# Kernel optimization log

Measured on AMD Instinct MI355X. Metric: run time of the kernel, lower is better.

Reference implementation:

```python
import jax, jax.numpy as jnp
import numpy as np

NUM_FEATURES = 128   # conv spatial length
WINDOW = 128         # conv channels / lstm seq len
KC = 16              # kernels per group
KS = 3               # conv kernel size
FC1 = 32             # number of independent LSTMs
H = 32               # lstm hidden size
NL = 2               # lstm layers
PAD = 1
POOL_LEN = (NUM_FEATURES + 2 * PAD) // 2  # maxpool(k=2,s=2,p=1) output length
B = 128


def setup_inputs():
    key = jax.random.key(0)
    ks = jax.random.split(key, 13)
    x = jax.random.normal(ks[0], (B, WINDOW, NUM_FEATURES), jnp.float32)
    conv_w = jax.random.normal(ks[1], (WINDOW * KC, 1, KS), jnp.float32) * 0.3
    conv_b = jax.random.normal(ks[2], (WINDOW * KC,), jnp.float32) * 0.1
    fc1_in = KC * POOL_LEN
    fc1_w = jax.random.normal(ks[3], (FC1, fc1_in), jnp.float32) * 0.02
    fc1_b = jax.random.normal(ks[4], (FC1,), jnp.float32) * 0.02
    w_ih0 = jax.random.normal(ks[5], (FC1, 4 * H), jnp.float32) * 0.1          # layer0, input size 1
    w_ih1 = jax.random.normal(ks[6], (NL - 1, FC1, 4 * H, H), jnp.float32) * 0.1
    w_hh = jax.random.normal(ks[7], (NL, FC1, 4 * H, H), jnp.float32) * 0.1
    b_lstm = jax.random.normal(ks[8], (NL, FC1, 4 * H), jnp.float32) * 0.1     # bias_ih + bias_hh combined
    mu_w = jax.random.normal(ks[9], (1, FC1 * H), jnp.float32) * 0.05
    mu_b = jax.random.normal(ks[10], (1,), jnp.float32) * 0.05
    lv_w = jax.random.normal(ks[11], (1, FC1 * H), jnp.float32) * 0.05
    lv_b = jax.random.normal(ks[12], (1,), jnp.float32) * 0.05
    return {"x": x, "conv_w": conv_w, "conv_b": conv_b, "fc1_w": fc1_w, "fc1_b": fc1_b,
            "w_ih0": w_ih0, "w_ih1": w_ih1, "w_hh": w_hh, "b_lstm": b_lstm,
            "mu_w": mu_w, "mu_b": mu_b, "lv_w": lv_w, "lv_b": lv_b}


def _lstm_cell(gates, c_prev):
    # torch gate order: i, f, g, o
    i, f, g, o = jnp.split(gates, 4, axis=-1)
    c_new = jax.nn.sigmoid(f) * c_prev + jax.nn.sigmoid(i) * jnp.tanh(g)
    h_new = jax.nn.sigmoid(o) * jnp.tanh(c_new)
    return h_new, c_new


def reference(x, conv_w, conv_b, fc1_w, fc1_b, w_ih0, w_ih1, w_hh, b_lstm, mu_w, mu_b, lv_w, lv_b):
    bsz = x.shape[0]
    # grouped conv1d: groups = WINDOW, each group maps 1 -> KC channels
    y = jax.lax.conv_general_dilated(x, conv_w, window_strides=(1,), padding=[(PAD, PAD)],
                                     feature_group_count=WINDOW,
                                     dimension_numbers=('NCH', 'OIH', 'NCH'))
    y = jax.nn.relu(y + conv_b[None, :, None])
    neg = jnp.finfo(y.dtype).min
    y = jnp.pad(y, ((0, 0), (0, 0), (PAD, PAD)), constant_values=neg)
    y = y.reshape(bsz, WINDOW * KC, POOL_LEN, 2).max(axis=-1)
    # regroup to [B, WINDOW, KC*POOL_LEN] (channel layout = group-major, matches torch view)
    y = y.reshape(bsz, WINDOW, KC * POOL_LEN)
    z = jnp.einsum('bwi,oi->bwo', y, fc1_w) + fc1_b   # [B, WINDOW, FC1]

    # FC1 independent NL-layer LSTMs batched over the feature axis; time axis = WINDOW
    h0 = jnp.zeros((NL, bsz, FC1, H), z.dtype)
    c0 = jnp.zeros_like(h0)

    def step(carry, x_t):  # x_t: [B, FC1]
        h, c = carry
        hs, cs = [], []
        gates = jnp.einsum('bf,fg->bfg', x_t, w_ih0) + jnp.einsum('bfh,fgh->bfg', h[0], w_hh[0]) + b_lstm[0]
        h_l, c_l = _lstm_cell(gates, c[0])
        hs.append(h_l); cs.append(c_l)
        for l in range(1, NL):
            gates = (jnp.einsum('bfh,fgh->bfg', h_l, w_ih1[l - 1])
                     + jnp.einsum('bfh,fgh->bfg', h[l], w_hh[l]) + b_lstm[l])
            h_l, c_l = _lstm_cell(gates, c[l])
            hs.append(h_l); cs.append(c_l)
        return (jnp.stack(hs), jnp.stack(cs)), None

    (h_fin, _), _ = jax.lax.scan(step, (h0, c0), jnp.transpose(z, (1, 0, 2)))
    combined = h_fin[-1].reshape(bsz, FC1 * H)  # top layer, last step; feature-major like torch.cat
    mu = combined @ mu_w.T + mu_b
    log_var = combined @ lv_w.T + lv_b
    sigma = jnp.exp(0.5 * log_var)
    return (mu - 1.96 * sigma, mu, mu + 1.96 * sigma, log_var)
```

## Files before the change

### kernel.cpp

```cpp
#include <hip/hip_runtime.h>
#include <hip/hip_bf16.h>
#include <math.h>

#define BATCH 128
#define WIN   128
#define NF    128
#define KC    16
#define POOL  65
#define NFC1  32
#define HS    32
#define LW    40
#define KP    1056
#define PSTR  1064

typedef float f32x4 __attribute__((ext_vector_type(4)));
typedef short bf16x8 __attribute__((ext_vector_type(8)));

#define LOG2E   1.442695041f
#define LOG2E2  2.885390082f

__device__ __forceinline__ float cellf(float& c, float gi, float gf, float gg, float go) {
    float ei = __builtin_amdgcn_exp2f(gi);
    float ef = __builtin_amdgcn_exp2f(gf);
    float eg = __builtin_amdgcn_exp2f(gg);
    float eo = __builtin_amdgcn_exp2f(go);
    float sf = __builtin_amdgcn_rcpf(1.f + ef);
    c = fmaf(sf, c, (eg - 1.f) * __builtin_amdgcn_rcpf((1.f + ei) * (eg + 1.f)));
    float ec = __builtin_amdgcn_exp2f(__builtin_amdgcn_fmed3f(c, -30.f, 30.f) * LOG2E2);
    return (ec - 1.f) * __builtin_amdgcn_rcpf((1.f + eo) * (ec + 1.f));
}
__device__ __forceinline__ unsigned short f2bf(float x) {
    __hip_bfloat16 h = __float2bfloat16(x);
    unsigned short u; __builtin_memcpy(&u, &h, 2); return u;
}
__device__ __forceinline__ float bf2f(unsigned short u) {
    unsigned int v = ((unsigned int)u) << 16;
    float f; __builtin_memcpy(&f, &v, 4); return f;
}
__device__ __forceinline__ bf16x8 load_row8_scaled(const float* row, float sc) {
    float4 lo = ((const float4*)row)[0];
    float4 hi = ((const float4*)row)[1];
    union { bf16x8 v; unsigned short u[8]; } t;
    t.u[0] = f2bf(lo.x * sc); t.u[1] = f2bf(lo.y * sc); t.u[2] = f2bf(lo.z * sc); t.u[3] = f2bf(lo.w * sc);
    t.u[4] = f2bf(hi.x * sc); t.u[5] = f2bf(hi.y * sc); t.u[6] = f2bf(hi.z * sc); t.u[7] = f2bf(hi.w * sc);
    return t.v;
}

__global__ __launch_bounds__(256) void k0_wconv(
    const float* __restrict__ fc1_w, unsigned short* __restrict__ w_bf)
{
    const int o = blockIdx.x;
    for (int i = threadIdx.x; i < KP; i += 256) {
        float v = (i < KC * POOL) ? fc1_w[(size_t)o * (KC * POOL) + i] : 0.f;
        w_bf[(size_t)o * KP + i] = f2bf(v);
    }
}

__global__ __launch_bounds__(128, 2) void k1_conv_fc1(
    const float* __restrict__ x, const float* __restrict__ conv_w, const float* __restrict__ conv_b,
    const unsigned short* __restrict__ w_bf, const float* __restrict__ fc1_b, float* __restrict__ z)
{
    __shared__ __align__(16) unsigned short xp[16][132];
    __shared__ __align__(16) unsigned short poolb[16 * PSTR];
    __shared__ float cw[KC][3];
    __shared__ float cb[KC];
    __shared__ float fb[NFC1];

    const int w = blockIdx.x >> 3;
    const int bbase = (blockIdx.x & 7) * 16;
    const int tid = threadIdx.x;

    if (tid < KC * 3) cw[tid / 3][tid % 3] = conv_w[(w * KC + tid / 3) * 3 + tid % 3];
    if (tid >= 64 && tid < 64 + KC) cb[tid - 64] = conv_b[w * KC + (tid - 64)];
    if (tid >= 96 && tid < 96 + NFC1) fb[tid - 96] = fc1_b[tid - 96];

    for (int i = tid; i < 16 * 32; i += 128) {
        int b = i >> 5, q = i & 31;
        float4 v = ((const float4*)(x + (size_t)(bbase + b) * (WIN * NF) + (size_t)w * NF))[q];
        unsigned short* dst = &xp[b][1 + q * 4];
        dst[0] = f2bf(v.x); dst[1] = f2bf(v.y); dst[2] = f2bf(v.z); dst[3] = f2bf(v.w);
    }
    if (tid < 16) { xp[tid][0] = 0; xp[tid][129] = 0; xp[tid][130] = 0; xp[tid][131] = 0; }
    __syncthreads();

    {
        const int b0 = tid >> 4;
        const int k = tid & 15;
        const float w0 = cw[k][0], w1 = cw[k][1], w2 = cw[k][2], bb = cb[k];
        #pragma unroll
        for (int half = 0; half < 2; ++half) {
            const int b = b0 + half * 8;
            float v1 = 0.f;
            float v2 = bf2f(xp[b][0]);
            float v3 = bf2f(xp[b][1]);
            unsigned short* prow = &poolb[b * PSTR + k * POOL];
            #pragma unroll 5
            for (int j = 0; j < POOL; ++j) {
                float v0 = v1; v1 = v2; v2 = v3;
                v3 = bf2f(xp[b][2 * j + 2]);
                float oa = bb + w0 * v0 + w1 * v1 + w2 * v2;
                float ob = bb + w0 * v1 + w1 * v2 + w2 * v3;
                float m = 0.f;
                if (j > 0)        m = fmaxf(m, oa);
                if (j < POOL - 1) m = fmaxf(m, ob);
                prow[j] = f2bf(m);
            }
        }
    }
    for (int i = tid; i < 16 * (KP - KC * POOL); i += 128) {
        int b = i >> 4, c = i & 15;
        poolb[b * PSTR + KC * POOL + c] = 0;
    }
    __syncthreads();

    const int lane = tid & 63;
    const int wid = tid >> 6;
    const int col = lane & 15;
    const int kg = lane >> 4;
    const int g = wid * 16 + col;
    f32x4 acc;
    {
        float bias = fb[g];
        acc[0] = bias; acc[1] = bias; acc[2] = bias; acc[3] = bias;
    }
    const unsigned short* wrow = w_bf + (size_t)g * KP;
    #pragma unroll 4
    for (int ks = 0; ks < KP / 32; ++ks) {
        bf16x8 aP = *(const bf16x8*)&poolb[col * PSTR + ks * 32 + kg * 8];
        bf16x8 bW = *(const bf16x8*)&wrow[ks * 32 + kg * 8];
        acc = __builtin_amdgcn_mfma_f32_16x16x32_bf16(aP, bW, acc, 0, 0, 0);
    }
    float4 st; st.x = acc[0]; st.y = acc[1]; st.z = acc[2]; st.w = acc[3];
    *(float4*)&z[(size_t)w * (NFC1 * BATCH) + (size_t)g * BATCH + bbase + kg * 4] = st;
}

__global__ __launch_bounds__(256, 1) void k2_lstm_mfma(
    const float* __restrict__ w_ih0, const float* __restrict__ w_ih1,
    const float* __restrict__ w_hh, const float* __restrict__ b_lstm,
    const float* __restrict__ z, float* __restrict__ h1fin)
{
    __shared__ float zs[WIN][16];
    __shared__ __align__(16) unsigned short h0b0[16 * LW];
    __shared__ __align__(16) unsigned short h0b1[16 * LW];
    __shared__ __align__(16) unsigned short h1b0[16 * LW];
    __shared__ __align__(16) unsigned short h1b1[16 * LW];

    const int f = blockIdx.x >> 3;
    const int bbase = (blockIdx.x & 7) * 16;
    const int tid = threadIdx.x;
    const int wid = tid >> 6, lane = tid & 63;
    const bool isL0 = (wid < 2);
    const int s = wid & 1;
    const int col = lane & 15;
    const int kg = lane >> 4;

    for (int i = tid; i < WIN * 4; i += 256) {
        int t = i >> 2, q = i & 3;
        ((float4*)&zs[t][0])[q] = ((const float4*)&z[(size_t)t * (NFC1 * BATCH) + f * BATCH + bbase])[q];
    }
    for (int i = tid; i < 16 * LW; i += 256) {
        h0b0[i] = 0; h0b1[i] = 0; h1b0[i] = 0; h1b1[i] = 0;
    }

    const float gsc[4] = { -LOG2E, -LOG2E, LOG2E2, -LOG2E };

    const float* WA = isL0 ? (w_hh + (size_t)f * 4096)
                           : (w_ih1 + (size_t)f * 4096);
    const float* WV = w_hh + (size_t)(NFC1 + f) * 4096;
    bf16x8 fA[4], fB[4];
    float bias[4], wi0[4];
    const int loff = isL0 ? 0 : (NFC1 * 128);
    #pragma unroll
    for (int gi = 0; gi < 4; ++gi) {
        int nt = gi * 2 + s;
        int g = nt * 16 + col;
        fA[gi] = load_row8_scaled(WA + g * 32 + kg * 8, gsc[gi]);
        if (!isL0) fB[gi] = load_row8_scaled(WV + g * 32 + kg * 8, gsc[gi]);
        bias[gi] = b_lstm[loff + f * 128 + g] * gsc[gi];
        wi0[gi] = w_ih0[f * 128 + g] * gsc[gi];
    }
    __syncthreads();

    const int hread = col * LW + kg * 8;
    const int hw0 = (kg * 4 + 0) * LW + 16 * s + col;
    float cst[4] = {0.f, 0.f, 0.f, 0.f};
    f32x4 zv = *(const f32x4*)&zs[0][kg * 4];

    auto body = [&](int it, const unsigned short* h0r, unsigned short* h0w,
                            const unsigned short* h1r, unsigned short* h1w) {
        if (isL0) {
            if (it < WIN) {
                bf16x8 hA = *(const bf16x8*)&h0r[hread];
                f32x4 aI, aF, aG, aO;
                #pragma unroll
                for (int j = 0; j < 4; ++j) {
                    aI[j] = fmaf(zv[j], wi0[0], bias[0]);
                    aF[j] = fmaf(zv[j], wi0[1], bias[1]);
                    aG[j] = fmaf(zv[j], wi0[2], bias[2]);
                    aO[j] = fmaf(zv[j], wi0[3], bias[3]);
                }
                aI = __builtin_amdgcn_mfma_f32_16x16x32_bf16(hA, fA[0], aI, 0, 0, 0);
                aF = __builtin_amdgcn_mfma_f32_16x16x32_bf16(hA, fA[1], aF, 0, 0, 0);
                aG = __builtin_amdgcn_mfma_f32_16x16x32_bf16(hA, fA[2], aG, 0, 0, 0);
                aO = __builtin_amdgcn_mfma_f32_16x16x32_bf16(hA, fA[3], aO, 0, 0, 0);
                if (it + 1 < WIN) zv = *(const f32x4*)&zs[it + 1][kg * 4];
                #pragma unroll
                for (int j = 0; j < 4; ++j) {
                    float h = cellf(cst[j], aI[j], aF[j], aG[j], aO[j]);
                    h0w[hw0 + j * LW] = f2bf(h);
                }
            }
        } else {
            if (it >= 1) {
                bf16x8 hA = *(const bf16x8*)&h0r[hread];
                bf16x8 hB = *(const bf16x8*)&h1r[hread];
                f32x4 aI, aF, aG, aO;
                #pragma unroll
                for (int j = 0; j < 4; ++j) { aI[j] = bias[0]; aF[j] = bias[1]; aG[j] = bias[2]; aO[j] = bias[3]; }
                aI = __builtin_amdgcn_mfma_f32_16x16x32_bf16(hA, fA[0], aI, 0, 0, 0);
                aI = __builtin_amdgcn_mfma_f32_16x16x32_bf16(hB, fB[0], aI, 0, 0, 0);
                aF = __builtin_amdgcn_mfma_f32_16x16x32_bf16(hA, fA[1], aF, 0, 0, 0);
                aF = __builtin_amdgcn_mfma_f32_16x16x32_bf16(hB, fB[1], aF, 0, 0, 0);
                aG = __builtin_amdgcn_mfma_f32_16x16x32_bf16(hA, fA[2], aG, 0, 0, 0);
                aG = __builtin_amdgcn_mfma_f32_16x16x32_bf16(hB, fB[2], aG, 0, 0, 0);
                aO = __builtin_amdgcn_mfma_f32_16x16x32_bf16(hA, fA[3], aO, 0, 0, 0);
                aO = __builtin_amdgcn_mfma_f32_16x16x32_bf16(hB, fB[3], aO, 0, 0, 0);
                if (it < WIN) {
                    #pragma unroll
                    for (int j = 0; j < 4; ++j) {
                        float h = cellf(cst[j], aI[j], aF[j], aG[j], aO[j]);
                        h1w[hw0 + j * LW] = f2bf(h);
                    }
                } else {
                    #pragma unroll
                    for (int j = 0; j < 4; ++j) {
                        float h = cellf(cst[j], aI[j], aF[j], aG[j], aO[j]);
                        h1fin[(size_t)(bbase + kg * 4 + j) * (NFC1 * HS) + f * HS + 16 * s + col] = h;
                    }
                }
            }
        }
    };

    body(0, h0b0, h0b1, h1b0, h1b1);
    __syncthreads();
    #pragma unroll 1
    for (int it = 1; it <= WIN; it += 2) {
        body(it,     h0b1, h0b0, h1b1, h1b0);
        __syncthreads();
        body(it + 1, h0b0, h0b1, h1b0, h1b1);
        __syncthreads();
    }
}

__global__ __launch_bounds__(128) void k3_head(
    const float* __restrict__ h1fin, const float* __restrict__ mu_w, const float* __restrict__ mu_b,
    const float* __restrict__ lv_w, const float* __restrict__ lv_b, float* __restrict__ out)
{
    const int b = blockIdx.x, tid = threadIdx.x;
    const float* hrow = h1fin + (size_t)b * (NFC1 * HS);
    float am = 0.f, al = 0.f;
    for (int i = tid; i < NFC1 * HS; i += 128) {
        float h = hrow[i];
        am = fmaf(h, mu_w[i], am);
        al = fmaf(h, lv_w[i], al);
    }
    for (int off = 32; off >= 1; off >>= 1) {
        am += __shfl_down(am, off, 64);
        al += __shfl_down(al, off, 64);
    }
    __shared__ float sm[2], sl[2];
    const int wv = tid >> 6, ln = tid & 63;
    if (ln == 0) { sm[wv] = am; sl[wv] = al; }
    __syncthreads();
    if (tid == 0) {
        float mu = sm[0] + sm[1] + mu_b[0];
        float lv = sl[0] + sl[1] + lv_b[0];
        float sg = expf(0.5f * lv);
        out[b]           = mu - 1.96f * sg;
        out[128 + b]     = mu;
        out[256 + b]     = mu + 1.96f * sg;
        out[384 + b]     = lv;
    }
}

extern "C" void kernel_launch(void* const* d_in, const int* in_sizes, int n_in,
                              void* d_out, int out_size, void* d_ws, size_t ws_size,
                              hipStream_t stream)
{
    const float* x      = (const float*)d_in[0];
    const float* conv_w = (const float*)d_in[1];
    const float* conv_b = (const float*)d_in[2];
    const float* fc1_w  = (const float*)d_in[3];
    const float* fc1_b  = (const float*)d_in[4];
    const float* w_ih0  = (const float*)d_in[5];
    const float* w_ih1  = (const float*)d_in[6];
    const float* w_hh   = (const float*)d_in[7];
    const float* b_lstm = (const float*)d_in[8];
    const float* mu_w   = (const float*)d_in[9];
    const float* mu_b   = (const float*)d_in[10];
    const float* lv_w   = (const float*)d_in[11];
    const float* lv_b   = (const float*)d_in[12];
    float* out = (float*)d_out;

    float* z     = (float*)d_ws;
    float* h1fin = z + (size_t)WIN * NFC1 * BATCH;
    unsigned short* w_bf = (unsigned short*)(h1fin + (size_t)BATCH * NFC1 * HS);

    k0_wconv<<<dim3(NFC1), dim3(256), 0, stream>>>(fc1_w, w_bf);
    k1_conv_fc1<<<dim3(WIN * 8), dim3(128), 0, stream>>>(x, conv_w, conv_b, w_bf, fc1_b, z);
    k2_lstm_mfma<<<dim3(NFC1 * 8), dim3(256), 0, stream>>>(w_ih0, w_ih1, w_hh, b_lstm, z, h1fin);
    k3_head<<<dim3(BATCH), dim3(128), 0, stream>>>(h1fin, mu_w, mu_b, lv_w, lv_b, out);
}
```

Baseline: 86.44 us.

## Pack two LSTM work units per 512-thread block in k2

The LSTM kernel now runs two independent (feature, batch-slice) units inside one 512-thread block, each with its own shared-memory z and h buffers, and launches half as many blocks. On a 256-CU MI355X the old 256 blocks of 256 threads already fit one per CU, so this halves the number of CUs in use while putting 8 waves per CU. The intent is likely to let one group's MFMA and transcendental latency hide behind the other's. In exchange the block-wide __syncthreads now couples both units, so each step waits on the slower group.

```diff
diff --git a/kernel.cpp b/kernel.cpp
--- a/kernel.cpp
+++ b/kernel.cpp
@@ -134,32 +134,35 @@
     *(float4*)&z[(size_t)w * (NFC1 * BATCH) + (size_t)g * BATCH + bbase + kg * 4] = st;
 }
 
-__global__ __launch_bounds__(256, 1) void k2_lstm_mfma(
+__global__ __launch_bounds__(512, 1) void k2_lstm_mfma(
     const float* __restrict__ w_ih0, const float* __restrict__ w_ih1,
     const float* __restrict__ w_hh, const float* __restrict__ b_lstm,
     const float* __restrict__ z, float* __restrict__ h1fin)
 {
-    __shared__ float zs[WIN][16];
-    __shared__ __align__(16) unsigned short h0b0[16 * LW];
-    __shared__ __align__(16) unsigned short h0b1[16 * LW];
-    __shared__ __align__(16) unsigned short h1b0[16 * LW];
-    __shared__ __align__(16) unsigned short h1b1[16 * LW];
-
-    const int f = blockIdx.x >> 3;
-    const int bbase = (blockIdx.x & 7) * 16;
+    __shared__ float zs[2][WIN][16];
+    __shared__ __align__(16) unsigned short h0b0[2][16 * LW];
+    __shared__ __align__(16) unsigned short h0b1[2][16 * LW];
+    __shared__ __align__(16) unsigned short h1b0[2][16 * LW];
+    __shared__ __align__(16) unsigned short h1b1[2][16 * LW];
+
     const int tid = threadIdx.x;
-    const int wid = tid >> 6, lane = tid & 63;
+    const int grp = tid >> 8;
+    const int gtid = tid & 255;
+    const int unit = blockIdx.x * 2 + grp;
+    const int f = unit >> 3;
+    const int bbase = (unit & 7) * 16;
+    const int wid = gtid >> 6, lane = gtid & 63;
     const bool isL0 = (wid < 2);
     const int s = wid & 1;
     const int col = lane & 15;
     const int kg = lane >> 4;
 
-    for (int i = tid; i < WIN * 4; i += 256) {
+    for (int i = gtid; i < WIN * 4; i += 256) {
         int t = i >> 2, q = i & 3;
-        ((float4*)&zs[t][0])[q] = ((const float4*)&z[(size_t)t * (NFC1 * BATCH) + f * BATCH + bbase])[q];
-    }
-    for (int i = tid; i < 16 * LW; i += 256) {
-        h0b0[i] = 0; h0b1[i] = 0; h1b0[i] = 0; h1b1[i] = 0;
+        ((float4*)&zs[grp][t][0])[q] = ((const float4*)&z[(size_t)t * (NFC1 * BATCH) + f * BATCH + bbase])[q];
+    }
+    for (int i = gtid; i < 16 * LW; i += 256) {
+        h0b0[grp][i] = 0; h0b1[grp][i] = 0; h1b0[grp][i] = 0; h1b1[grp][i] = 0;
     }
 
     const float gsc[4] = { -LOG2E, -LOG2E, LOG2E2, -LOG2E };
@@ -184,7 +187,12 @@
     const int hread = col * LW + kg * 8;
     const int hw0 = (kg * 4 + 0) * LW + 16 * s + col;
     float cst[4] = {0.f, 0.f, 0.f, 0.f};
-    f32x4 zv = *(const f32x4*)&zs[0][kg * 4];
+    f32x4 zv = *(const f32x4*)&zs[grp][0][kg * 4];
+
+    const unsigned short* B0r = &h0b0[grp][0];
+    unsigned short*       B0w = &h0b1[grp][0];
+    const unsigned short* B1r = &h1b0[grp][0];
+    unsigned short*       B1w = &h1b1[grp][0];
 
     auto body = [&](int it, const unsigned short* h0r, unsigned short* h0w,
                             const unsigned short* h1r, unsigned short* h1w) {
@@ -203,7 +211,7 @@
                 aF = __builtin_amdgcn_mfma_f32_16x16x32_bf16(hA, fA[1], aF, 0, 0, 0);
                 aG = __builtin_amdgcn_mfma_f32_16x16x32_bf16(hA, fA[2], aG, 0, 0, 0);
                 aO = __builtin_amdgcn_mfma_f32_16x16x32_bf16(hA, fA[3], aO, 0, 0, 0);
-                if (it + 1 < WIN) zv = *(const f32x4*)&zs[it + 1][kg * 4];
+                if (it + 1 < WIN) zv = *(const f32x4*)&zs[grp][it + 1][kg * 4];
                 #pragma unroll
                 for (int j = 0; j < 4; ++j) {
                     float h = cellf(cst[j], aI[j], aF[j], aG[j], aO[j]);
@@ -242,13 +250,13 @@
         }
     };
 
-    body(0, h0b0, h0b1, h1b0, h1b1);
+    body(0, B0r, B0w, B1r, B1w);
     __syncthreads();
     #pragma unroll 1
     for (int it = 1; it <= WIN; it += 2) {
-        body(it,     h0b1, h0b0, h1b1, h1b0);
+        body(it,     B0w, (unsigned short*)B0r, B1w, (unsigned short*)B1r);
         __syncthreads();
-        body(it + 1, h0b0, h0b1, h1b0, h1b1);
+        body(it + 1, B0r, B0w, B1r, B1w);
         __syncthreads();
     }
 }
@@ -309,6 +317,6 @@
 
     k0_wconv<<<dim3(NFC1), dim3(256), 0, stream>>>(fc1_w, w_bf);
     k1_conv_fc1<<<dim3(WIN * 8), dim3(128), 0, stream>>>(x, conv_w, conv_b, w_bf, fc1_b, z);
-    k2_lstm_mfma<<<dim3(NFC1 * 8), dim3(256), 0, stream>>>(w_ih0, w_ih1, w_hh, b_lstm, z, h1fin);
+    k2_lstm_mfma<<<dim3(NFC1 * 8 / 2), dim3(512), 0, stream>>>(w_ih0, w_ih1, w_hh, b_lstm, z, h1fin);
     k3_head<<<dim3(BATCH), dim3(128), 0, stream>>>(h1fin, mu_w, mu_b, lv_w, lv_b, out);
 }
```

Result: slower. 112.2 us (+29.8%).
